# Kernel tuning notes

Hardware: AMD Instinct MI355X
Metric: run time of the kernel (lower is better)

Reference implementation:

```python
import jax, jax.numpy as jnp
import numpy as np

B, L, H, NH = 32, 512, 512, 8
HD = H // NH
SCALE = HD ** -0.5


def _heads(x):
    # (B, L, H) -> (B, NH, L, HD)
    return x.reshape(B, L, NH, HD).transpose(0, 2, 1, 3)


def _score(x, Wq, bq, Wk, bk):
    Q = _heads(x @ Wq.T + bq)
    K = _heads(x @ Wk.T + bk)
    return jnp.einsum('bhqd,bhkd->bhqk', Q, K) * SCALE


def setup_inputs() -> dict:
    key = jax.random.key(0)
    ks = jax.random.split(key, 16)
    d = {
        'seq_id': jax.random.normal(ks[0], (B, L, H), jnp.float32),
        'side_cate': jax.random.normal(ks[1], (B, L, H), jnp.float32),
        'side_brand': jax.random.normal(ks[2], (B, L, H), jnp.float32),
        'V_id_input': jax.random.normal(ks[3], (B, L, H), jnp.float32),
        'relative_time': jax.random.normal(ks[4], (B, NH, L, L), jnp.float32) * 0.02,
        'attn_mask': jnp.broadcast_to(jnp.tril(jnp.ones((L, L), bool)), (B, L, L)),
    }
    s = (2.0 / H) ** 0.5
    names = ['q_id', 'k_id', 'v', 'q_cate', 'k_cate', 'q_brand', 'k_brand', 'o']
    for i, n in enumerate(names):
        d['W' + n] = jax.random.normal(ks[5 + i], (H, H), jnp.float32) * s
        d['b' + n] = jnp.zeros((H,), jnp.float32)
    return d


def reference(seq_id, side_cate, side_brand, V_id_input, relative_time, attn_mask,
              Wq_id, bq_id, Wk_id, bk_id, Wv, bv,
              Wq_cate, bq_cate, Wk_cate, bk_cate,
              Wq_brand, bq_brand, Wk_brand, bk_brand,
              Wo, bo):
    V = _heads(V_id_input @ Wv.T + bv)  # (B, NH, L, HD)
    total = _score(seq_id, Wq_id, bq_id, Wk_id, bk_id)
    total = total + _score(side_cate, Wq_cate, bq_cate, Wk_cate, bk_cate)
    total = total + _score(side_brand, Wq_brand, bq_brand, Wk_brand, bk_brand)
    total = total + relative_time
    total = jnp.where(attn_mask[:, None], total, -jnp.inf)
    w = jax.nn.softmax(total.astype(jnp.float32), axis=-1).astype(total.dtype)
    w = jnp.nan_to_num(w, nan=0.0)
    # eval mode: dropout is identity
    attn_out = jnp.einsum('bhqk,bhkd->bhqd', w, V)
    attn_out = attn_out.transpose(0, 2, 1, 3).reshape(B, L, H)
    return attn_out @ Wo.T + bo
```

## Files before the change

kernel.cpp:

```cpp
#include <hip/hip_runtime.h>
#include <hip/hip_bf16.h>
#include <stdint.h>


typedef __bf16 bf16x8 __attribute__((ext_vector_type(8)));
typedef float f32x4 __attribute__((ext_vector_type(4)));

#define LOG2E 1.4426950408889634f

__device__ int g_isf32;
__device__ __align__(16) unsigned short g_Wbf[8 * 512 * 512];
__device__ __align__(16) unsigned short g_Xbv[32 * 512 * 512];

__device__ __forceinline__ f32x4 mfma16(bf16x8 a, bf16x8 b, f32x4 c) {
    return __builtin_amdgcn_mfma_f32_16x16x32_bf16(a, b, c, 0, 0, 0);
}

__device__ __forceinline__ float qmax16(float x) {
    x = fmaxf(x, __shfl_xor(x, 1));
    x = fmaxf(x, __shfl_xor(x, 2));
    x = fmaxf(x, __shfl_xor(x, 4));
    x = fmaxf(x, __shfl_xor(x, 8));
    return x;
}
__device__ __forceinline__ float qsum16(float x) {
    x += __shfl_xor(x, 1);
    x += __shfl_xor(x, 2);
    x += __shfl_xor(x, 4);
    x += __shfl_xor(x, 8);
    return x;
}

__device__ __forceinline__ float ldf(const void* p, size_t off, int isf) {
    return isf ? ((const float*)p)[off]
               : __bfloat162float(((const __hip_bfloat16*)p)[off]);
}

__device__ __forceinline__ void glds16(const void* g, void* l) {
    __builtin_amdgcn_global_load_lds(
        (const __attribute__((address_space(1))) void*)g,
        (__attribute__((address_space(3))) void*)l, 16, 0, 0);
}

__global__ void sniff_kernel(const unsigned short* __restrict__ p) {
    int t = threadIdx.x;
    int bad = 0, zc = 0;
    #pragma unroll
    for (int i = 0; i < 32; i++) {
        unsigned short u = p[(t * 32 + i) * 2];
        int e = (u >> 7) & 0xFF;
        bad |= (e >= 0xF0);
        zc += (u == 0);
    }
    unsigned long long mb = __ballot(bad != 0);
    #pragma unroll
    for (int s = 1; s < 64; s <<= 1) zc += __shfl_xor(zc, s);
    if (t == 0) g_isf32 = (mb != 0ull || zc > 1024) ? 1 : 0;
}

__global__ __launch_bounds__(256) void conv4(
    const float* __restrict__ s0, const float* __restrict__ s1,
    const float* __restrict__ s2, const float* __restrict__ s3,
    __hip_bfloat16* __restrict__ d0, __hip_bfloat16* __restrict__ d1,
    __hip_bfloat16* __restrict__ d2)
{
    if (!g_isf32) return;
    const int z = blockIdx.z;
    const float* s = (z == 0) ? s0 : (z == 1) ? s1 : (z == 2) ? s2 : s3;
    __hip_bfloat16* d = (z == 0) ? d0 : (z == 1) ? d1 : (z == 2) ? d2
                                      : (__hip_bfloat16*)g_Xbv;
    const int N8 = 32 * 512 * 512 / 8;
    for (int i = blockIdx.x * 256 + threadIdx.x; i < N8; i += gridDim.x * 256) {
        f32x4 a = ((const f32x4*)s)[2 * i];
        f32x4 b = ((const f32x4*)s)[2 * i + 1];
        bf16x8 o;
        o[0] = (__bf16)a[0]; o[1] = (__bf16)a[1]; o[2] = (__bf16)a[2]; o[3] = (__bf16)a[3];
        o[4] = (__bf16)b[0]; o[5] = (__bf16)b[1]; o[6] = (__bf16)b[2]; o[7] = (__bf16)b[3];
        ((bf16x8*)d)[i] = o;
    }
}

__global__ __launch_bounds__(256) void convW(
    const float* __restrict__ W0, const float* __restrict__ W1,
    const float* __restrict__ W2, const float* __restrict__ W3,
    const float* __restrict__ W4, const float* __restrict__ W5,
    const float* __restrict__ W6, const float* __restrict__ Wo)
{
    if (!g_isf32) return;
    const int z = blockIdx.z;
    const float* src;
    switch (z) {
        case 0: src = W0; break; case 1: src = W1; break;
        case 2: src = W2; break; case 3: src = W3; break;
        case 4: src = W4; break; case 5: src = W5; break;
        case 6: src = W6; break; default: src = Wo; break;
    }
    int i = blockIdx.x * 256 + threadIdx.x;
    f32x4 a = ((const f32x4*)src)[2 * i];
    f32x4 b = ((const f32x4*)src)[2 * i + 1];
    bf16x8 o;
    o[0] = (__bf16)a[0]; o[1] = (__bf16)a[1]; o[2] = (__bf16)a[2]; o[3] = (__bf16)a[3];
    o[4] = (__bf16)b[0]; o[5] = (__bf16)b[1]; o[6] = (__bf16)b[2]; o[7] = (__bf16)b[3];
    ((bf16x8*)g_Wbf)[z * 32768 + i] = o;
}

__global__ __launch_bounds__(256, 2) void gemm_all(
    const void* __restrict__ xs, const void* __restrict__ xc,
    const void* __restrict__ xb, const void* __restrict__ xv,
    const __hip_bfloat16* __restrict__ Xbs, const __hip_bfloat16* __restrict__ Xbc,
    const __hip_bfloat16* __restrict__ Xbb,
    const void* __restrict__ W0, const void* __restrict__ B0,
    const void* __restrict__ W1, const void* __restrict__ B1,
    const void* __restrict__ W2, const void* __restrict__ B2,
    const void* __restrict__ W3, const void* __restrict__ B3,
    const void* __restrict__ W4, const void* __restrict__ B4,
    const void* __restrict__ W5, const void* __restrict__ B5,
    const void* __restrict__ W6, const void* __restrict__ B6,
    const void* __restrict__ Wo, const void* __restrict__ Bo,
    const __hip_bfloat16* __restrict__ AO,
    __hip_bfloat16* __restrict__ Qcat, __hip_bfloat16* __restrict__ Kcat,
    __hip_bfloat16* __restrict__ Vt, void* __restrict__ Out,
    int oproj)
{
    __shared__ __align__(16) __hip_bfloat16 As[2][128 * 64];
    __shared__ __align__(16) __hip_bfloat16 Bs[2][128 * 64];

    const int isf = g_isf32;
    const int t = threadIdx.x;
    const int lane = t & 63, w = t >> 6;
    const int ln = lane & 15, hi = lane >> 4;
    const int wm = w >> 1, wn = w & 1;
    const int tm = blockIdx.x * 128, tn = blockIdx.y * 128;

    const __hip_bfloat16* Ab;
    const void *W, *bias;
    int kind = 3, comp = 0, wslot = 7;
    if (oproj) {
        Ab = AO; W = Wo; bias = Bo;
    } else {
        switch (blockIdx.z) {
            case 0:  Ab = isf ? Xbs : (const __hip_bfloat16*)xs;
                     W = W0; bias = B0; kind = 0; comp = 0; wslot = 0; break;
            case 1:  Ab = isf ? Xbs : (const __hip_bfloat16*)xs;
                     W = W1; bias = B1; kind = 1; comp = 0; wslot = 1; break;
            case 2:  Ab = isf ? (const __hip_bfloat16*)g_Xbv : (const __hip_bfloat16*)xv;
                     W = W2; bias = B2; kind = 2; comp = 0; wslot = 2; break;
            case 3:  Ab = isf ? Xbc : (const __hip_bfloat16*)xc;
                     W = W3; bias = B3; kind = 0; comp = 1; wslot = 3; break;
            case 4:  Ab = isf ? Xbc : (const __hip_bfloat16*)xc;
                     W = W4; bias = B4; kind = 1; comp = 1; wslot = 4; break;
            case 5:  Ab = isf ? Xbb : (const __hip_bfloat16*)xb;
                     W = W5; bias = B5; kind = 0; comp = 2; wslot = 5; break;
            default: Ab = isf ? Xbb : (const __hip_bfloat16*)xb;
                     W = W6; bias = B6; kind = 1; comp = 2; wslot = 6; break;
        }
    }
    const __hip_bfloat16* Wb = isf ? (const __hip_bfloat16*)g_Wbf + (size_t)wslot * 262144
                                   : (const __hip_bfloat16*)W;

    const int csw = (((lane & 7) ^ ((lane >> 3) & 7)) * 8);
    const int rsub = (w * 8) + (lane >> 3);

    f32x4 acc[4][4] = {};

    #define STAGE(bi, kt)                                                        \
        do {                                                                     \
            int _k0 = (kt) * 64;                                                 \
            _Pragma("unroll")                                                    \
            for (int r = 0; r < 4; r++)                                          \
                glds16(Ab + (size_t)(tm + r * 32 + rsub) * 512 + _k0 + csw,      \
                       (char*)&As[bi][0] + r * 4096 + w * 1024);                 \
            _Pragma("unroll")                                                    \
            for (int r = 0; r < 4; r++)                                          \
                glds16(Wb + (size_t)(tn + r * 32 + rsub) * 512 + _k0 + csw,      \
                       (char*)&Bs[bi][0] + r * 4096 + w * 1024);                 \
        } while (0)

    STAGE(0, 0);
    STAGE(1, 1);
    asm volatile("s_waitcnt vmcnt(8)" ::: "memory");
    __builtin_amdgcn_s_barrier();

    for (int k = 0; k < 8; k++) {
        const int cur = k & 1;
        asm volatile("" ::: "memory");
        const __hip_bfloat16* Asc = &As[cur][0];
        const __hip_bfloat16* Bsc = &Bs[cur][0];
        #pragma unroll
        for (int kk = 0; kk < 64; kk += 32) {
            bf16x8 af[4], bfr[4];
            #pragma unroll
            for (int i = 0; i < 4; i++)
                af[i] = *(const bf16x8*)&Asc[(wm * 64 + i * 16 + ln) * 64 +
                                             ((kk + hi * 8) ^ ((ln & 7) * 8))];
            #pragma unroll
            for (int j = 0; j < 4; j++)
                bfr[j] = *(const bf16x8*)&Bsc[(wn * 64 + j * 16 + ln) * 64 +
                                              ((kk + hi * 8) ^ ((ln & 7) * 8))];
            #pragma unroll
            for (int i = 0; i < 4; i++)
                #pragma unroll
                for (int j = 0; j < 4; j++)
                    acc[i][j] = mfma16(af[i], bfr[j], acc[i][j]);
        }
        __builtin_amdgcn_s_barrier();
        if (k + 2 < 8) {
            STAGE(cur, k + 2);
            asm volatile("s_waitcnt vmcnt(8)" ::: "memory");
        } else {
            asm volatile("s_waitcnt vmcnt(0)" ::: "memory");
        }
        __builtin_amdgcn_s_barrier();
    }
    #undef STAGE

    #pragma unroll
    for (int j = 0; j < 4; j++) {
        int col = tn + wn * 64 + j * 16 + ln;
        float bv = ldf(bias, col, isf);
        int h = col >> 6, d = col & 63;
        #pragma unroll
        for (int i = 0; i < 4; i++) {
            #pragma unroll
            for (int r = 0; r < 4; r++) {
                int row = tm + wm * 64 + i * 16 + hi * 4 + r;
                float val = acc[i][j][r] + bv;
                int b = row >> 9, l = row & 511;
                if (kind == 0)
                    Qcat[((size_t)(b * 8 + h) * 512 + l) * 192 + comp * 64 + d] =
                        __float2bfloat16(val);
                else if (kind == 1)
                    Kcat[((size_t)(b * 8 + h) * 512 + l) * 192 + comp * 64 + d] =
                        __float2bfloat16(val);
                else if (kind == 2)
                    Vt[((size_t)(b * 8 + h) * 64 + d) * 512 + l] =
                        __float2bfloat16(val);
                else if (isf)
                    ((float*)Out)[(size_t)row * 512 + col] = val;
                else
                    ((__hip_bfloat16*)Out)[(size_t)row * 512 + col] =
                        __float2bfloat16(val);
            }
        }
    }
}

__global__ __launch_bounds__(256, 2) void attn_kernel(
    const __hip_bfloat16* __restrict__ Qcat,
    const __hip_bfloat16* __restrict__ Kcat,
    const __hip_bfloat16* __restrict__ Vt,
    const void* __restrict__ rel,
    __hip_bfloat16* __restrict__ AO)
{
    __shared__ __align__(16) __hip_bfloat16 Ks[64 * 200];
    __shared__ __align__(16) __hip_bfloat16 Vs[64 * 72];
    __shared__ __align__(16) __hip_bfloat16 Ps[4 * 32 * 72];

    const int isf = g_isf32;
    const int t = threadIdx.x;
    const int lane = t & 63, w = t >> 6;
    const int ln = lane & 15, hi = lane >> 4;
    const int qt = blockIdx.x, h = blockIdx.y, b = blockIdx.z;
    const int qb = qt * 128;
    const size_t bh = (size_t)(b * 8 + h);

    const __hip_bfloat16* qc = Qcat + bh * 512 * 192;
    const __hip_bfloat16* kc = Kcat + bh * 512 * 192;
    const __hip_bfloat16* vp = Vt + bh * 64 * 512;
    const size_t rbase = bh * 512 * 512;

    bf16x8 qf[2][6];
    #pragma unroll
    for (int i = 0; i < 2; i++)
        #pragma unroll
        for (int kf = 0; kf < 6; kf++)
            qf[i][kf] = *(const bf16x8*)(qc + (size_t)(qb + w * 32 + i * 16 + ln) * 192
                                            + kf * 32 + hi * 8);

    float mst[2][4], lst[2][4];
    f32x4 oacc[2][4] = {};
    #pragma unroll
    for (int i = 0; i < 2; i++)
        #pragma unroll
        for (int r = 0; r < 4; r++) { mst[i][r] = -1e30f; lst[i][r] = 0.f; }

    const int nkt = 2 * qt + 2;
    for (int kt = 0; kt < nkt; kt++) {
        const int kb = kt * 64;
        __syncthreads();

        #pragma unroll
        for (int r = 0; r < 6; r++) {
            int e = r * 2048 + t * 8;
            int row = e / 192, col = e - row * 192;
            bf16x8 v = *(const bf16x8*)(kc + (size_t)(kb + row) * 192 + col);
            *(bf16x8*)&Ks[row * 200 + col] = v;
        }
        #pragma unroll
        for (int r = 0; r < 2; r++) {
            int e = r * 2048 + t * 8;
            int row = e >> 6, col = e & 63;
            bf16x8 v = *(const bf16x8*)(vp + (size_t)row * 512 + kb + col);
            *(bf16x8*)&Vs[row * 72 + col] = v;
        }
        __syncthreads();

        f32x4 s[2][4] = {};
        __builtin_amdgcn_s_setprio(1);
        #pragma unroll
        for (int kf = 0; kf < 6; kf++) {
            bf16x8 bfr[4];
            #pragma unroll
            for (int j = 0; j < 4; j++)
                bfr[j] = *(const bf16x8*)&Ks[(j * 16 + ln) * 200 + kf * 32 + hi * 8];
            #pragma unroll
            for (int i = 0; i < 2; i++)
                #pragma unroll
                for (int j = 0; j < 4; j++)
                    s[i][j] = mfma16(qf[i][kf], bfr[j], s[i][j]);
        }
        __builtin_amdgcn_s_setprio(0);

        #pragma unroll
        for (int i = 0; i < 2; i++) {
            #pragma unroll
            for (int r = 0; r < 4; r++) {
                int qrow = qb + w * 32 + i * 16 + hi * 4 + r;
                size_t roff = rbase + (size_t)qrow * 512 + kb;
                #pragma unroll
                for (int j = 0; j < 4; j++) {
                    int col = kb + j * 16 + ln;
                    float rv = ldf(rel, roff + j * 16 + ln, isf);
                    float v = fmaf(s[i][j][r], 0.125f * LOG2E, rv * LOG2E);
                    s[i][j][r] = (col > qrow) ? -1e30f : v;
                }
            }
        }

        #pragma unroll
        for (int i = 0; i < 2; i++) {
            #pragma unroll
            for (int r = 0; r < 4; r++) {
                float mx = fmaxf(fmaxf(s[i][0][r], s[i][1][r]),
                                 fmaxf(s[i][2][r], s[i][3][r]));
                mx = qmax16(mx);
                float mnew = fmaxf(mst[i][r], mx);
                float al = exp2f(mst[i][r] - mnew);
                float sum = 0.f;
                #pragma unroll
                for (int j = 0; j < 4; j++) {
                    float p = exp2f(s[i][j][r] - mnew);
                    s[i][j][r] = p;
                    sum += p;
                }
                sum = qsum16(sum);
                lst[i][r] = lst[i][r] * al + sum;
                mst[i][r] = mnew;
                #pragma unroll
                for (int jn = 0; jn < 4; jn++)
                    oacc[i][jn][r] *= al;
            }
        }

        __hip_bfloat16* pw = &Ps[w * 32 * 72];
        #pragma unroll
        for (int i = 0; i < 2; i++) {
            #pragma unroll
            for (int r = 0; r < 4; r++) {
                int prow = i * 16 + hi * 4 + r;
                #pragma unroll
                for (int j = 0; j < 4; j++)
                    pw[prow * 72 + j * 16 + ln] = __float2bfloat16(s[i][j][r]);
            }
        }
        __syncthreads();

        __builtin_amdgcn_s_setprio(1);
        #pragma unroll
        for (int kk = 0; kk < 64; kk += 32) {
            bf16x8 ap[2], bv[4];
            #pragma unroll
            for (int i = 0; i < 2; i++)
                ap[i] = *(const bf16x8*)&Ps[w * 2304 + (i * 16 + ln) * 72 + kk + hi * 8];
            #pragma unroll
            for (int jn = 0; jn < 4; jn++)
                bv[jn] = *(const bf16x8*)&Vs[(jn * 16 + ln) * 72 + kk + hi * 8];
            #pragma unroll
            for (int i = 0; i < 2; i++)
                #pragma unroll
                for (int jn = 0; jn < 4; jn++)
                    oacc[i][jn] = mfma16(ap[i], bv[jn], oacc[i][jn]);
        }
        __builtin_amdgcn_s_setprio(0);
    }

    #pragma unroll
    for (int i = 0; i < 2; i++) {
        #pragma unroll
        for (int r = 0; r < 4; r++) {
            int qrow = qb + w * 32 + i * 16 + hi * 4 + r;
            float inv = 1.0f / lst[i][r];
            __hip_bfloat16* orow = AO + ((size_t)(b * 512 + qrow)) * 512 + h * 64;
            #pragma unroll
            for (int jn = 0; jn < 4; jn++)
                orow[jn * 16 + ln] = __float2bfloat16(oacc[i][jn][r] * inv);
        }
    }
}

extern "C" void kernel_launch(void* const* d_in, const int* in_sizes, int n_in,
                              void* d_out, int out_size, void* d_ws, size_t ws_size,
                              hipStream_t stream) {
    (void)in_sizes; (void)n_in; (void)out_size; (void)ws_size;
    const void* xs  = d_in[0];
    const void* xc  = d_in[1];
    const void* xb  = d_in[2];
    const void* xv  = d_in[3];
    const void* rel = d_in[4];
    const void* W0 = d_in[6];    const void* B0 = d_in[7];
    const void* W1 = d_in[8];    const void* B1 = d_in[9];
    const void* W2 = d_in[10];   const void* B2 = d_in[11];
    const void* W3 = d_in[12];   const void* B3 = d_in[13];
    const void* W4 = d_in[14];   const void* B4 = d_in[15];
    const void* W5 = d_in[16];   const void* B5 = d_in[17];
    const void* W6 = d_in[18];   const void* B6 = d_in[19];
    const void* Wo = d_in[20];   const void* Bo = d_in[21];

    char* ws = (char*)d_ws;
    __hip_bfloat16* Qcat = (__hip_bfloat16*)(ws);
    __hip_bfloat16* Kcat = (__hip_bfloat16*)(ws + 50331648);
    __hip_bfloat16* Vt   = (__hip_bfloat16*)(ws + 100663296);
    __hip_bfloat16* AO   = (__hip_bfloat16*)(ws + 117440512);

    __hip_bfloat16* Xbs = AO;
    __hip_bfloat16* Xbc = (__hip_bfloat16*)d_out;
    __hip_bfloat16* Xbb = (__hip_bfloat16*)((char*)d_out + 16777216);

    dim3 blk(256, 1, 1);
    sniff_kernel<<<1, 64, 0, stream>>>((const unsigned short*)xs);
    conv4<<<dim3(1024, 1, 4), blk, 0, stream>>>(
        (const float*)xs, (const float*)xc, (const float*)xb, (const float*)xv,
        Xbs, Xbc, Xbb);
    convW<<<dim3(128, 1, 8), blk, 0, stream>>>(
        (const float*)W0, (const float*)W1, (const float*)W2, (const float*)W3,
        (const float*)W4, (const float*)W5, (const float*)W6, (const float*)Wo);
    gemm_all<<<dim3(128, 4, 7), blk, 0, stream>>>(
        xs, xc, xb, xv, Xbs, Xbc, Xbb,
        W0, B0, W1, B1, W2, B2, W3, B3, W4, B4, W5, B5, W6, B6,
        Wo, Bo, AO, Qcat, Kcat, Vt, d_out, 0);
    attn_kernel<<<dim3(4, 8, 32), blk, 0, stream>>>(Qcat, Kcat, Vt, rel, AO);
    gemm_all<<<dim3(128, 4, 1), blk, 0, stream>>>(
        xs, xc, xb, xv, Xbs, Xbc, Xbb,
        W0, B0, W1, B1, W2, B2, W3, B3, W4, B4, W5, B5, W6, B6,
        Wo, Bo, AO, Qcat, Kcat, Vt, d_out, 1);
}
```

Measured before the change: 682.0 us.

## Replace double-buffered GEMM pipeline with single buffer and higher occupancy

Result: no change. 679.9 us (-0.3%).

```diff
diff --git a/kernel.cpp b/kernel.cpp
--- a/kernel.cpp
+++ b/kernel.cpp
@@ -104,7 +104,7 @@
     ((bf16x8*)g_Wbf)[z * 32768 + i] = o;
 }
 
-__global__ __launch_bounds__(256, 2) void gemm_all(
+__global__ __launch_bounds__(256, 4) void gemm_all(
     const void* __restrict__ xs, const void* __restrict__ xc,
     const void* __restrict__ xb, const void* __restrict__ xv,
     const __hip_bfloat16* __restrict__ Xbs, const __hip_bfloat16* __restrict__ Xbc,
@@ -122,8 +122,8 @@
     __hip_bfloat16* __restrict__ Vt, void* __restrict__ Out,
     int oproj)
 {
-    __shared__ __align__(16) __hip_bfloat16 As[2][128 * 64];
-    __shared__ __align__(16) __hip_bfloat16 Bs[2][128 * 64];
+    __shared__ __align__(16) __hip_bfloat16 As[128 * 64];
+    __shared__ __align__(16) __hip_bfloat16 Bs[128 * 64];
 
     const int isf = g_isf32;
     const int t = threadIdx.x;
@@ -163,56 +163,36 @@
 
     f32x4 acc[4][4] = {};
 
-    #define STAGE(bi, kt)                                                        \
-        do {                                                                     \
-            int _k0 = (kt) * 64;                                                 \
-            _Pragma("unroll")                                                    \
-            for (int r = 0; r < 4; r++)                                          \
-                glds16(Ab + (size_t)(tm + r * 32 + rsub) * 512 + _k0 + csw,      \
-                       (char*)&As[bi][0] + r * 4096 + w * 1024);                 \
-            _Pragma("unroll")                                                    \
-            for (int r = 0; r < 4; r++)                                          \
-                glds16(Wb + (size_t)(tn + r * 32 + rsub) * 512 + _k0 + csw,      \
-                       (char*)&Bs[bi][0] + r * 4096 + w * 1024);                 \
-        } while (0)
-
-    STAGE(0, 0);
-    STAGE(1, 1);
-    asm volatile("s_waitcnt vmcnt(8)" ::: "memory");
-    __builtin_amdgcn_s_barrier();
-
-    for (int k = 0; k < 8; k++) {
-        const int cur = k & 1;
-        asm volatile("" ::: "memory");
-        const __hip_bfloat16* Asc = &As[cur][0];
-        const __hip_bfloat16* Bsc = &Bs[cur][0];
+    for (int k0 = 0; k0 < 512; k0 += 64) {
+        #pragma unroll
+        for (int r = 0; r < 4; r++)
+            glds16(Ab + (size_t)(tm + r * 32 + rsub) * 512 + k0 + csw,
+                   (char*)As + r * 4096 + w * 1024);
+        #pragma unroll
+        for (int r = 0; r < 4; r++)
+            glds16(Wb + (size_t)(tn + r * 32 + rsub) * 512 + k0 + csw,
+                   (char*)Bs + r * 4096 + w * 1024);
+        __syncthreads();
+
         #pragma unroll
         for (int kk = 0; kk < 64; kk += 32) {
             bf16x8 af[4], bfr[4];
             #pragma unroll
             for (int i = 0; i < 4; i++)
-                af[i] = *(const bf16x8*)&Asc[(wm * 64 + i * 16 + ln) * 64 +
+                af[i] = *(const bf16x8*)&As[(wm * 64 + i * 16 + ln) * 64 +
+                                            ((kk + hi * 8) ^ ((ln & 7) * 8))];
+            #pragma unroll
+            for (int j = 0; j < 4; j++)
+                bfr[j] = *(const bf16x8*)&Bs[(wn * 64 + j * 16 + ln) * 64 +
                                              ((kk + hi * 8) ^ ((ln & 7) * 8))];
-            #pragma unroll
-            for (int j = 0; j < 4; j++)
-                bfr[j] = *(const bf16x8*)&Bsc[(wn * 64 + j * 16 + ln) * 64 +
-                                              ((kk + hi * 8) ^ ((ln & 7) * 8))];
             #pragma unroll
             for (int i = 0; i < 4; i++)
                 #pragma unroll
                 for (int j = 0; j < 4; j++)
                     acc[i][j] = mfma16(af[i], bfr[j], acc[i][j]);
         }
-        __builtin_amdgcn_s_barrier();
-        if (k + 2 < 8) {
-            STAGE(cur, k + 2);
-            asm volatile("s_waitcnt vmcnt(8)" ::: "memory");
-        } else {
-            asm volatile("s_waitcnt vmcnt(0)" ::: "memory");
-        }
-        __builtin_amdgcn_s_barrier();
-    }
-    #undef STAGE
+        __syncthreads();
+    }
 
     #pragma unroll
     for (int j = 0; j < 4; j++) {
```
